# Optimization experiments

Hardware: AMD Instinct MI355X
Metric: run time of the kernel (lower is better)

The kernel has to match this reference:

```python
import jax, jax.numpy as jnp
import numpy as np

EPS = 1e-5


def adder_conv(x, w, stride, padding):
    """AdderNet conv: out[n,o,i,j] = -sum_k |patch[n,i,j,k] - w[o,k]|.
    x: [N, Cin, H, W], w: [Cout, Cin, kh, kw]."""
    Cout, Cin, kh, kw = w.shape
    # patches: [N, Cin*kh*kw, Ho, Wo]
    p = jax.lax.conv_general_dilated_patches(
        x, (kh, kw), (stride, stride), [(padding, padding), (padding, padding)])
    p = jnp.transpose(p, (0, 2, 3, 1))  # [N, Ho, Wo, K]
    wf = w.reshape(Cout, Cin * kh * kw)  # [Cout, K]
    # sequential map over output channels bounds peak memory to one [N,Ho,Wo,K]
    # abs-diff tensor at a time (no huge [N,Cout,Ho,Wo,K] broadcast)
    def one_out(wo):
        return jnp.sum(jnp.abs(p - wo), axis=-1)  # [N, Ho, Wo]
    out = jax.lax.map(one_out, wf)  # [Cout, N, Ho, Wo]
    return -jnp.transpose(out, (1, 0, 2, 3))  # [N, Cout, Ho, Wo]


def bn_relu6(x, gamma, beta):
    # training-mode BatchNorm2d (batch statistics, biased variance) + ReLU6
    mean = jnp.mean(x, axis=(0, 2, 3), keepdims=True)
    var = jnp.var(x, axis=(0, 2, 3), keepdims=True)
    y = (x - mean) * jax.lax.rsqrt(var + EPS)
    y = y * gamma.reshape(1, -1, 1, 1) + beta.reshape(1, -1, 1, 1)
    return jnp.clip(y, 0.0, 6.0)


def setup_inputs() -> dict:
    key = jax.random.key(0)
    ks = jax.random.split(key, 20)
    f32 = jnp.float32

    def wgt(k, shape):
        return jax.random.normal(k, shape, f32) * 0.05

    def bn(k, c):
        k1, k2 = jax.random.split(k)
        g = 1.0 + 0.1 * jax.random.normal(k1, (c,), f32)
        b = 0.1 * jax.random.normal(k2, (c,), f32)
        return g, b

    x = jax.random.normal(ks[0], (16, 512, 38, 38), f32)
    w1 = wgt(ks[1], (256, 512, 1, 1)); g1, b1 = bn(ks[7], 256)
    w2 = wgt(ks[2], (512, 256, 3, 3)); g2, b2 = bn(ks[8], 512)
    w3 = wgt(ks[3], (128, 512, 1, 1)); g3, b3 = bn(ks[9], 128)
    w4 = wgt(ks[4], (256, 128, 3, 3)); g4, b4 = bn(ks[10], 256)
    w5 = wgt(ks[5], (128, 256, 1, 1)); g5, b5 = bn(ks[11], 128)
    w6 = wgt(ks[6], (256, 128, 3, 3)); g6, b6 = bn(ks[12], 256)
    return {"x": x,
            "w1": w1, "g1": g1, "b1": b1,
            "w2": w2, "g2": g2, "b2": b2,
            "w3": w3, "g3": g3, "b3": b3,
            "w4": w4, "g4": g4, "b4": b4,
            "w5": w5, "g5": g5, "b5": b5,
            "w6": w6, "g6": g6, "b6": b6}


def reference(x, w1, g1, b1, w2, g2, b2, w3, g3, b3,
              w4, g4, b4, w5, g5, b5, w6, g6, b6):
    x = bn_relu6(adder_conv(x, w1, 1, 0), g1, b1)  # [N,256,38,38]
    x = bn_relu6(adder_conv(x, w2, 2, 1), g2, b2)  # [N,512,19,19]
    x = bn_relu6(adder_conv(x, w3, 1, 0), g3, b3)  # [N,128,19,19]
    x = bn_relu6(adder_conv(x, w4, 2, 1), g4, b4)  # [N,256,10,10]
    x = bn_relu6(adder_conv(x, w5, 1, 0), g5, b5)  # [N,128,10,10]
    x = bn_relu6(adder_conv(x, w6, 2, 0), g6, b6)  # [N,256,4,4]
    return x
```

## Files before the change

kernel.cpp:

```cpp
#include <hip/hip_runtime.h>


#define QSCALE 131072.0f
#define QBIAS  1048576.5f
#define QINV   7.62939453125e-06

template <bool IS3x3, bool BN>
__global__ __launch_bounds__(256, 4)
void adder_conv(const float* __restrict__ x, const unsigned* __restrict__ wT,
                const float2* __restrict__ ab, unsigned* __restrict__ part,
                int Cin, int H, int W, int Wo, int Cout,
                int stride, int pad, int cpz, int P, int PI, int Pp)
{
    constexpr int KC = 32;
    __shared__ unsigned xs[KC][68];
    __shared__ unsigned ws[KC][128];
    __shared__ float2 abls[512];

    const int t  = threadIdx.x;
    const int tx = t & 15, ty = t >> 4;
    const int ptile = blockIdx.x * 64, otile = blockIdx.y * 128;
    const int pp = t & 63, rg = t >> 6;
    const int oq = t & 31, kr = t >> 5;

    if (BN) {
        for (int i = t; i < Cin; i += 256) abls[i] = ab[i];
        __syncthreads();
    }

    const int p_st = ptile + pp;
    const bool pv = p_st < P;
    int n_st = 0, q = 0;
    if (pv) { n_st = p_st / PI; q = p_st - n_st * PI; }
    const int oh = q / Wo, ow = q - oh * Wo;
    const int ih0 = oh * stride - pad, iw0 = ow * stride - pad;
    const int HWi = H * W;
    const float* xb = x + (size_t)n_st * Cin * HWi;
    const unsigned* wbase = wT + otile + oq * 4;

    unsigned acc[4][8] = {};

    const int chunkBeg = blockIdx.z * cpz, chunkEnd = chunkBeg + cpz;

    float xr0, xr1, xr2, xr3, xr4, xr5, xr6, xr7;
    uint4 wr0, wr1, wr2, wr3;
    int c0P = 0; bool vP = false;

#define ISSUE(CH) do {                                                        \
        const int k0_ = (CH) * KC;                                            \
        int c0_, ih_, iw_;                                                    \
        if (IS3x3) {                                                          \
            const int tap_ = k0_ / Cin;               \
            c0_ = k0_ - tap_ * Cin;                                           \
            const int kh_ = tap_ / 3, kw_ = tap_ - kh_ * 3;                   \
            ih_ = ih0 + kh_; iw_ = iw0 + kw_;                                 \
        } else { c0_ = k0_; ih_ = ih0; iw_ = iw0; }                           \
        vP = pv && (!IS3x3 || (ih_ >= 0 && ih_ < H && iw_ >= 0 && iw_ < W));  \
        c0P = c0_;                                                            \
        const float* px_ = xb + (size_t)(c0_ + rg) * HWi + (ih_ * W + iw_);   \
        xr0 = vP ? px_[0] : 0.f;                                              \
        xr1 = vP ? px_[(size_t) 4 * HWi] : 0.f;                               \
        xr2 = vP ? px_[(size_t) 8 * HWi] : 0.f;                               \
        xr3 = vP ? px_[(size_t)12 * HWi] : 0.f;                               \
        xr4 = vP ? px_[(size_t)16 * HWi] : 0.f;                               \
        xr5 = vP ? px_[(size_t)20 * HWi] : 0.f;                               \
        xr6 = vP ? px_[(size_t)24 * HWi] : 0.f;                               \
        xr7 = vP ? px_[(size_t)28 * HWi] : 0.f;                               \
        const unsigned* pw_ = wbase + (size_t)(k0_ + kr) * Cout;              \
        wr0 = *(const uint4*)(pw_);                                           \
        wr1 = *(const uint4*)(pw_ + (size_t) 8 * Cout);                       \
        wr2 = *(const uint4*)(pw_ + (size_t)16 * Cout);                       \
        wr3 = *(const uint4*)(pw_ + (size_t)24 * Cout);                       \
    } while (0)

#define BNQ(V, J, DST)                                                        \
        {                                                                     \
            float vv_ = V;                                                    \
            if (BN) {                                                         \
                const float2 s_ = abls[c0P + rg + 4 * (J)];                   \
                vv_ = fminf(fmaxf(fmaf(s_.x, vv_, s_.y), 0.f), 6.f);          \
                vv_ = vP ? vv_ : 0.f;            \
            }                                                                 \
            DST = (unsigned)fmaf(vv_, QSCALE, QBIAS);                         \
        }

#define WRITE_LDS() do {                                                      \
        unsigned q0_, q1_, q2_, q3_, q4_, q5_, q6_, q7_;                      \
        BNQ(xr0, 0, q0_) BNQ(xr1, 1, q1_) BNQ(xr2, 2, q2_) BNQ(xr3, 3, q3_)   \
        BNQ(xr4, 4, q4_) BNQ(xr5, 5, q5_) BNQ(xr6, 6, q6_) BNQ(xr7, 7, q7_)   \
        xs[rg     ][pp] = q0_; xs[rg +  4][pp] = q1_;                         \
        xs[rg +  8][pp] = q2_; xs[rg + 12][pp] = q3_;                         \
        xs[rg + 16][pp] = q4_; xs[rg + 20][pp] = q5_;                         \
        xs[rg + 24][pp] = q6_; xs[rg + 28][pp] = q7_;                         \
        *(uint4*)&ws[kr     ][oq * 4] = wr0;                                  \
        *(uint4*)&ws[kr +  8][oq * 4] = wr1;                                  \
        *(uint4*)&ws[kr + 16][oq * 4] = wr2;                                  \
        *(uint4*)&ws[kr + 24][oq * 4] = wr3;                                  \
    } while (0)

    ISSUE(chunkBeg);

    for (int ch = chunkBeg; ch < chunkEnd; ++ch) {
        WRITE_LDS();
        if (ch + 1 < chunkEnd) ISSUE(ch + 1);
        asm volatile("s_waitcnt lgkmcnt(0)" ::: "memory");
        __builtin_amdgcn_s_barrier();
        asm volatile("" ::: "memory");

#pragma unroll 2
        for (int kk = 0; kk < KC; ++kk) {
            const uint4 xv = *(const uint4*)&xs[kk][tx * 4];
            const uint4 wa = *(const uint4*)&ws[kk][ty * 8];
            const uint4 wb = *(const uint4*)&ws[kk][ty * 8 + 4];
#define S1(A, XC, WC) asm("v_sad_u32 %0, %1, %2, %0" : "+v"(A) : "v"(XC), "v"(WC));
#define SROW(I, XC)                                             \
            S1(acc[I][0], XC, wa.x) S1(acc[I][1], XC, wa.y)     \
            S1(acc[I][2], XC, wa.z) S1(acc[I][3], XC, wa.w)     \
            S1(acc[I][4], XC, wb.x) S1(acc[I][5], XC, wb.y)     \
            S1(acc[I][6], XC, wb.z) S1(acc[I][7], XC, wb.w)
            SROW(0, xv.x) SROW(1, xv.y) SROW(2, xv.z) SROW(3, xv.w)
#undef SROW
#undef S1
        }
        asm volatile("" ::: "memory");
        __builtin_amdgcn_s_barrier();
        asm volatile("" ::: "memory");
    }
#undef ISSUE
#undef BNQ
#undef WRITE_LDS

    const int p0 = ptile + tx * 4;
    const bool full = (p0 + 3) < P;
#pragma unroll
    for (int jj = 0; jj < 8; ++jj) {
        const int o = otile + ty * 8 + jj;
        unsigned* dst = part + ((size_t)blockIdx.z * Cout + o) * Pp + p0;
        if (full) {
            *(uint4*)dst = make_uint4(acc[0][jj], acc[1][jj], acc[2][jj], acc[3][jj]);
        } else {
#pragma unroll
            for (int i = 0; i < 4; ++i)
                if (p0 + i < P) dst[i] = acc[i][jj];
        }
    }
}

__global__ void combine_stats(const unsigned* __restrict__ part, float* __restrict__ fin,
                              double* __restrict__ st, int C, int PI, int Z, int Pp)
{
    const int c = blockIdx.x, n = blockIdx.y, t = threadIdx.x;
    const int pbase = n * PI;
    double s = 0.0, s2 = 0.0;
    for (int qq = t; qq < PI; qq += 256) {
        unsigned long long u = 0;
        for (int z = 0; z < Z; ++z)
            u += part[((size_t)z * C + c) * Pp + pbase + qq];
        const float v = -(float)((double)u * QINV);
        fin[((size_t)n * C + c) * PI + qq] = v;
        s += v; s2 += (double)v * v;
    }
    __shared__ double sh[256], sh2[256];
    sh[t] = s; sh2[t] = s2; __syncthreads();
    for (int off = 128; off > 0; off >>= 1) {
        if (t < off) { sh[t] += sh[t + off]; sh2[t] += sh2[t + off]; }
        __syncthreads();
    }
    if (t == 0) {
        unsafeAtomicAdd(&st[2 * c], sh[0]);
        unsafeAtomicAdd(&st[2 * c + 1], sh2[0]);
    }
}

__global__ void ab_kernel(const double* __restrict__ st, const float* __restrict__ gamma,
                          const float* __restrict__ beta, float2* __restrict__ ab,
                          int C, double invCount)
{
    const int c = blockIdx.x * blockDim.x + threadIdx.x;
    if (c < C) {
        const double mean = st[2 * c] * invCount;
        const double var  = st[2 * c + 1] * invCount - mean * mean;
        const float a = gamma[c] * rsqrtf((float)var + 1e-5f);
        const float b = beta[c] - (float)mean * a;
        ab[c] = make_float2(a, b);
    }
}

__global__ void apply_kernel(const float* __restrict__ y, const float2* __restrict__ ab,
                             float* __restrict__ out, int total, int C, int PI)
{
    const int i = blockIdx.x * 256 + threadIdx.x;
    if (i < total) {
        const int c = (i / PI) % C;
        const float2 s = ab[c];
        out[i] = fminf(fmaxf(fmaf(s.x, y[i], s.y), 0.f), 6.f);
    }
}

struct TDesc { const float* w; unsigned* wT; int Cout; int Cin; int Tap; int elems; };
struct TPack { TDesc d[6]; };

__global__ void transpose_all(TPack p)
{
    const TDesc d = p.d[blockIdx.y];
    const int i = blockIdx.x * 256 + threadIdx.x;
    if (i < d.elems) {
        const int k = i / d.Cout, o = i - k * d.Cout;
        const int tap = k / d.Cin, c = k - tap * d.Cin;
        const float v = d.w[((size_t)o * d.Cin + c) * d.Tap + tap];
        d.wT[i] = (unsigned)fmaf(v, QSCALE, QBIAS);
    }
}

extern "C" void kernel_launch(void* const* d_in, const int* in_sizes, int n_in,
                              void* d_out, int out_size, void* d_ws, size_t ws_size,
                              hipStream_t stream)
{
    const float* x = (const float*)d_in[0];
    const float *w[6], *g[6], *bt[6];
    for (int i = 0; i < 6; ++i) {
        w[i]  = (const float*)d_in[1 + 3 * i];
        g[i]  = (const float*)d_in[2 + 3 * i];
        bt[i] = (const float*)d_in[3 + 3 * i];
    }

    char* ws = (char*)d_ws;
    float* bufA = (float*)ws;
    float* bufB = (float*)(ws + 23658496);
    unsigned* part = (unsigned*)(ws + 23658496 + 11829248);
    size_t off = 23658496 + 11829248 + 23658496;
    const int wElems[6] = {256 * 512, 512 * 2304, 128 * 512,
                           256 * 1152, 128 * 256, 256 * 1152};
    unsigned* wT[6];
    for (int i = 0; i < 6; ++i) { wT[i] = (unsigned*)(ws + off); off += (size_t)wElems[i] * 4; }
    double* st = (double*)(ws + off); off += 3072 * 8;
    float2* ab = (float2*)(ws + off);
    const int stOff[6] = {0, 512, 1536, 1792, 2304, 2560};
    const int abOff[6] = {0, 256, 768, 896, 1152, 1280};

    const dim3 blk(256);

    hipMemsetAsync(st, 0, 3072 * 8, stream);

    TPack tp;
    const int wCout[6] = {256, 512, 128, 256, 128, 256};
    const int wCin[6]  = {512, 256, 512, 128, 256, 128};
    const int wTap[6]  = {1, 9, 1, 9, 1, 9};
    for (int i = 0; i < 6; ++i)
        tp.d[i] = TDesc{w[i], wT[i], wCout[i], wCin[i], wTap[i], wElems[i]};
    transpose_all<<<dim3((1179648 + 255) / 256, 6), blk, 0, stream>>>(tp);

    adder_conv<false, false><<<dim3(361, 2, 1), blk, 0, stream>>>(
        x, wT[0], nullptr, part, 512, 38, 38, 38, 256, 1, 0, 16, 23104, 1444, 23104);
    combine_stats<<<dim3(256, 16), blk, 0, stream>>>(part, bufA, st + stOff[0], 256, 1444, 1, 23104);
    ab_kernel<<<1, blk, 0, stream>>>(st + stOff[0], g[0], bt[0], ab + abOff[0], 256, 1.0 / 23104);

    adder_conv<true, true><<<dim3(91, 4, 2), blk, 0, stream>>>(
        bufA, wT[1], ab + abOff[0], part, 256, 38, 38, 19, 512, 2, 1, 36, 5776, 361, 5776);
    combine_stats<<<dim3(512, 16), blk, 0, stream>>>(part, bufB, st + stOff[1], 512, 361, 2, 5776);
    ab_kernel<<<2, blk, 0, stream>>>(st + stOff[1], g[1], bt[1], ab + abOff[1], 512, 1.0 / 5776);

    adder_conv<false, true><<<dim3(91, 1, 8), blk, 0, stream>>>(
        bufB, wT[2], ab + abOff[1], part, 512, 19, 19, 19, 128, 1, 0, 2, 5776, 361, 5776);
    combine_stats<<<dim3(128, 16), blk, 0, stream>>>(part, bufA, st + stOff[2], 128, 361, 8, 5776);
    ab_kernel<<<1, blk, 0, stream>>>(st + stOff[2], g[2], bt[2], ab + abOff[2], 128, 1.0 / 5776);

    adder_conv<true, true><<<dim3(25, 2, 12), blk, 0, stream>>>(
        bufA, wT[3], ab + abOff[2], part, 128, 19, 19, 10, 256, 2, 1, 3, 1600, 100, 1600);
    combine_stats<<<dim3(256, 16), blk, 0, stream>>>(part, bufB, st + stOff[3], 256, 100, 12, 1600);
    ab_kernel<<<1, blk, 0, stream>>>(st + stOff[3], g[3], bt[3], ab + abOff[3], 256, 1.0 / 1600);

    adder_conv<false, true><<<dim3(25, 1, 8), blk, 0, stream>>>(
        bufB, wT[4], ab + abOff[3], part, 256, 10, 10, 10, 128, 1, 0, 1, 1600, 100, 1600);
    combine_stats<<<dim3(128, 16), blk, 0, stream>>>(part, bufA, st + stOff[4], 128, 100, 8, 1600);
    ab_kernel<<<1, blk, 0, stream>>>(st + stOff[4], g[4], bt[4], ab + abOff[4], 128, 1.0 / 1600);

    adder_conv<true, true><<<dim3(4, 2, 18), blk, 0, stream>>>(
        bufA, wT[5], ab + abOff[4], part, 128, 10, 10, 4, 256, 2, 0, 2, 256, 16, 256);
    combine_stats<<<dim3(256, 16), blk, 0, stream>>>(part, bufB, st + stOff[5], 256, 16, 18, 256);
    ab_kernel<<<1, blk, 0, stream>>>(st + stOff[5], g[5], bt[5], ab + abOff[5], 256, 1.0 / 256);

    apply_kernel<<<(65536 + 255) / 256, blk, 0, stream>>>(bufB, ab + abOff[5], (float*)d_out,
                                                          65536, 256, 16);
}
```

Measured before the change: 668.8 us.

## Enlarge adder-conv pixel tile to 128 with split 2x4x8 register microtile

Doubles the pixel tile per block from 64 to 128 and gives each thread a 2x4x8 accumulator block built from two split x and w sub-tiles. This lowers the LDS reads per v_sad op and halves the grid size in the pixel dimension. The cost is more registers per thread (launch bounds lowered to 3 blocks), fewer blocks to fill the GPU, and more waste on the tail tiles of small layers.

```diff
diff --git a/kernel.cpp b/kernel.cpp
--- a/kernel.cpp
+++ b/kernel.cpp
@@ -6,21 +6,21 @@
 #define QINV   7.62939453125e-06
 
 template <bool IS3x3, bool BN>
-__global__ __launch_bounds__(256, 4)
+__global__ __launch_bounds__(256, 3)
 void adder_conv(const float* __restrict__ x, const unsigned* __restrict__ wT,
                 const float2* __restrict__ ab, unsigned* __restrict__ part,
                 int Cin, int H, int W, int Wo, int Cout,
                 int stride, int pad, int cpz, int P, int PI, int Pp)
 {
     constexpr int KC = 32;
-    __shared__ unsigned xs[KC][68];
+    __shared__ unsigned xs[KC][132];
     __shared__ unsigned ws[KC][128];
     __shared__ float2 abls[512];
 
     const int t  = threadIdx.x;
     const int tx = t & 15, ty = t >> 4;
-    const int ptile = blockIdx.x * 64, otile = blockIdx.y * 128;
-    const int pp = t & 63, rg = t >> 6;
+    const int ptile = blockIdx.x * 128, otile = blockIdx.y * 128;
+    const int pp = t & 127, rg = t >> 7;
     const int oq = t & 31, kr = t >> 5;
 
     if (BN) {
@@ -38,11 +38,12 @@
     const float* xb = x + (size_t)n_st * Cin * HWi;
     const unsigned* wbase = wT + otile + oq * 4;
 
-    unsigned acc[4][8] = {};
+    unsigned acc[2][4][8] = {};
 
     const int chunkBeg = blockIdx.z * cpz, chunkEnd = chunkBeg + cpz;
 
     float xr0, xr1, xr2, xr3, xr4, xr5, xr6, xr7;
+    float xr8, xr9, xr10, xr11, xr12, xr13, xr14, xr15;
     uint4 wr0, wr1, wr2, wr3;
     int c0P = 0; bool vP = false;
 
@@ -50,7 +51,7 @@
         const int k0_ = (CH) * KC;                                            \
         int c0_, ih_, iw_;                                                    \
         if (IS3x3) {                                                          \
-            const int tap_ = k0_ / Cin;               \
+            const int tap_ = k0_ / Cin;                \
             c0_ = k0_ - tap_ * Cin;                                           \
             const int kh_ = tap_ / 3, kw_ = tap_ - kh_ * 3;                   \
             ih_ = ih0 + kh_; iw_ = iw0 + kw_;                                 \
@@ -58,14 +59,22 @@
         vP = pv && (!IS3x3 || (ih_ >= 0 && ih_ < H && iw_ >= 0 && iw_ < W));  \
         c0P = c0_;                                                            \
         const float* px_ = xb + (size_t)(c0_ + rg) * HWi + (ih_ * W + iw_);   \
-        xr0 = vP ? px_[0] : 0.f;                                              \
-        xr1 = vP ? px_[(size_t) 4 * HWi] : 0.f;                               \
-        xr2 = vP ? px_[(size_t) 8 * HWi] : 0.f;                               \
-        xr3 = vP ? px_[(size_t)12 * HWi] : 0.f;                               \
-        xr4 = vP ? px_[(size_t)16 * HWi] : 0.f;                               \
-        xr5 = vP ? px_[(size_t)20 * HWi] : 0.f;                               \
-        xr6 = vP ? px_[(size_t)24 * HWi] : 0.f;                               \
-        xr7 = vP ? px_[(size_t)28 * HWi] : 0.f;                               \
+        xr0  = vP ? px_[0] : 0.f;                                             \
+        xr1  = vP ? px_[(size_t) 2 * HWi] : 0.f;                              \
+        xr2  = vP ? px_[(size_t) 4 * HWi] : 0.f;                              \
+        xr3  = vP ? px_[(size_t) 6 * HWi] : 0.f;                              \
+        xr4  = vP ? px_[(size_t) 8 * HWi] : 0.f;                              \
+        xr5  = vP ? px_[(size_t)10 * HWi] : 0.f;                              \
+        xr6  = vP ? px_[(size_t)12 * HWi] : 0.f;                              \
+        xr7  = vP ? px_[(size_t)14 * HWi] : 0.f;                              \
+        xr8  = vP ? px_[(size_t)16 * HWi] : 0.f;                              \
+        xr9  = vP ? px_[(size_t)18 * HWi] : 0.f;                              \
+        xr10 = vP ? px_[(size_t)20 * HWi] : 0.f;                              \
+        xr11 = vP ? px_[(size_t)22 * HWi] : 0.f;                              \
+        xr12 = vP ? px_[(size_t)24 * HWi] : 0.f;                              \
+        xr13 = vP ? px_[(size_t)26 * HWi] : 0.f;                              \
+        xr14 = vP ? px_[(size_t)28 * HWi] : 0.f;                              \
+        xr15 = vP ? px_[(size_t)30 * HWi] : 0.f;                              \
         const unsigned* pw_ = wbase + (size_t)(k0_ + kr) * Cout;              \
         wr0 = *(const uint4*)(pw_);                                           \
         wr1 = *(const uint4*)(pw_ + (size_t) 8 * Cout);                       \
@@ -77,7 +86,7 @@
         {                                                                     \
             float vv_ = V;                                                    \
             if (BN) {                                                         \
-                const float2 s_ = abls[c0P + rg + 4 * (J)];                   \
+                const float2 s_ = abls[c0P + rg + 2 * (J)];                   \
                 vv_ = fminf(fmaxf(fmaf(s_.x, vv_, s_.y), 0.f), 6.f);          \
                 vv_ = vP ? vv_ : 0.f;            \
             }                                                                 \
@@ -86,12 +95,19 @@
 
 #define WRITE_LDS() do {                                                      \
         unsigned q0_, q1_, q2_, q3_, q4_, q5_, q6_, q7_;                      \
-        BNQ(xr0, 0, q0_) BNQ(xr1, 1, q1_) BNQ(xr2, 2, q2_) BNQ(xr3, 3, q3_)   \
-        BNQ(xr4, 4, q4_) BNQ(xr5, 5, q5_) BNQ(xr6, 6, q6_) BNQ(xr7, 7, q7_)   \
-        xs[rg     ][pp] = q0_; xs[rg +  4][pp] = q1_;                         \
-        xs[rg +  8][pp] = q2_; xs[rg + 12][pp] = q3_;                         \
-        xs[rg + 16][pp] = q4_; xs[rg + 20][pp] = q5_;                         \
-        xs[rg + 24][pp] = q6_; xs[rg + 28][pp] = q7_;                         \
+        unsigned q8_, q9_, qA_, qB_, qC_, qD_, qE_, qF_;                      \
+        BNQ(xr0,  0, q0_) BNQ(xr1,  1, q1_) BNQ(xr2,  2, q2_) BNQ(xr3,  3, q3_) \
+        BNQ(xr4,  4, q4_) BNQ(xr5,  5, q5_) BNQ(xr6,  6, q6_) BNQ(xr7,  7, q7_) \
+        BNQ(xr8,  8, q8_) BNQ(xr9,  9, q9_) BNQ(xr10,10, qA_) BNQ(xr11,11, qB_) \
+        BNQ(xr12,12, qC_) BNQ(xr13,13, qD_) BNQ(xr14,14, qE_) BNQ(xr15,15, qF_) \
+        xs[rg     ][pp] = q0_; xs[rg +  2][pp] = q1_;                         \
+        xs[rg +  4][pp] = q2_; xs[rg +  6][pp] = q3_;                         \
+        xs[rg +  8][pp] = q4_; xs[rg + 10][pp] = q5_;                         \
+        xs[rg + 12][pp] = q6_; xs[rg + 14][pp] = q7_;                         \
+        xs[rg + 16][pp] = q8_; xs[rg + 18][pp] = q9_;                         \
+        xs[rg + 20][pp] = qA_; xs[rg + 22][pp] = qB_;                         \
+        xs[rg + 24][pp] = qC_; xs[rg + 26][pp] = qD_;                         \
+        xs[rg + 28][pp] = qE_; xs[rg + 30][pp] = qF_;                         \
         *(uint4*)&ws[kr     ][oq * 4] = wr0;                                  \
         *(uint4*)&ws[kr +  8][oq * 4] = wr1;                                  \
         *(uint4*)&ws[kr + 16][oq * 4] = wr2;                                  \
@@ -109,16 +125,18 @@
 
 #pragma unroll 2
         for (int kk = 0; kk < KC; ++kk) {
-            const uint4 xv = *(const uint4*)&xs[kk][tx * 4];
-            const uint4 wa = *(const uint4*)&ws[kk][ty * 8];
-            const uint4 wb = *(const uint4*)&ws[kk][ty * 8 + 4];
+            const uint4 xa = *(const uint4*)&xs[kk][tx * 4];
+            const uint4 xb2 = *(const uint4*)&xs[kk][64 + tx * 4];
+            const uint4 wa = *(const uint4*)&ws[kk][ty * 4];
+            const uint4 wb = *(const uint4*)&ws[kk][64 + ty * 4];
 #define S1(A, XC, WC) asm("v_sad_u32 %0, %1, %2, %0" : "+v"(A) : "v"(XC), "v"(WC));
-#define SROW(I, XC)                                             \
-            S1(acc[I][0], XC, wa.x) S1(acc[I][1], XC, wa.y)     \
-            S1(acc[I][2], XC, wa.z) S1(acc[I][3], XC, wa.w)     \
-            S1(acc[I][4], XC, wb.x) S1(acc[I][5], XC, wb.y)     \
-            S1(acc[I][6], XC, wb.z) S1(acc[I][7], XC, wb.w)
-            SROW(0, xv.x) SROW(1, xv.y) SROW(2, xv.z) SROW(3, xv.w)
+#define SROW(a, i, XC)                                            \
+            S1(acc[a][i][0], XC, wa.x) S1(acc[a][i][1], XC, wa.y) \
+            S1(acc[a][i][2], XC, wa.z) S1(acc[a][i][3], XC, wa.w) \
+            S1(acc[a][i][4], XC, wb.x) S1(acc[a][i][5], XC, wb.y) \
+            S1(acc[a][i][6], XC, wb.z) S1(acc[a][i][7], XC, wb.w)
+            SROW(0, 0, xa.x) SROW(0, 1, xa.y) SROW(0, 2, xa.z) SROW(0, 3, xa.w)
+            SROW(1, 0, xb2.x) SROW(1, 1, xb2.y) SROW(1, 2, xb2.z) SROW(1, 3, xb2.w)
 #undef SROW
 #undef S1
         }
@@ -130,18 +148,22 @@
 #undef BNQ
 #undef WRITE_LDS
 
-    const int p0 = ptile + tx * 4;
-    const bool full = (p0 + 3) < P;
 #pragma unroll
-    for (int jj = 0; jj < 8; ++jj) {
-        const int o = otile + ty * 8 + jj;
-        unsigned* dst = part + ((size_t)blockIdx.z * Cout + o) * Pp + p0;
-        if (full) {
-            *(uint4*)dst = make_uint4(acc[0][jj], acc[1][jj], acc[2][jj], acc[3][jj]);
-        } else {
+    for (int a = 0; a < 2; ++a) {
+        const int p0 = ptile + a * 64 + tx * 4;
+        const bool full = (p0 + 3) < P;
 #pragma unroll
-            for (int i = 0; i < 4; ++i)
-                if (p0 + i < P) dst[i] = acc[i][jj];
+        for (int jj = 0; jj < 8; ++jj) {
+            const int o = otile + (jj < 4 ? ty * 4 + jj : 64 + ty * 4 + (jj - 4));
+            unsigned* dst = part + ((size_t)blockIdx.z * Cout + o) * Pp + p0;
+            if (full) {
+                *(uint4*)dst = make_uint4(acc[a][0][jj], acc[a][1][jj],
+                                          acc[a][2][jj], acc[a][3][jj]);
+            } else {
+#pragma unroll
+                for (int i = 0; i < 4; ++i)
+                    if (p0 + i < P) dst[i] = acc[a][i][jj];
+            }
         }
     }
 }
@@ -250,32 +272,32 @@
         tp.d[i] = TDesc{w[i], wT[i], wCout[i], wCin[i], wTap[i], wElems[i]};
     transpose_all<<<dim3((1179648 + 255) / 256, 6), blk, 0, stream>>>(tp);
 
-    adder_conv<false, false><<<dim3(361, 2, 1), blk, 0, stream>>>(
+    adder_conv<false, false><<<dim3(181, 2, 1), blk, 0, stream>>>(
         x, wT[0], nullptr, part, 512, 38, 38, 38, 256, 1, 0, 16, 23104, 1444, 23104);
     combine_stats<<<dim3(256, 16), blk, 0, stream>>>(part, bufA, st + stOff[0], 256, 1444, 1, 23104);
     ab_kernel<<<1, blk, 0, stream>>>(st + stOff[0], g[0], bt[0], ab + abOff[0], 256, 1.0 / 23104);
 
-    adder_conv<true, true><<<dim3(91, 4, 2), blk, 0, stream>>>(
+    adder_conv<true, true><<<dim3(46, 4, 2), blk, 0, stream>>>(
         bufA, wT[1], ab + abOff[0], part, 256, 38, 38, 19, 512, 2, 1, 36, 5776, 361, 5776);
     combine_stats<<<dim3(512, 16), blk, 0, stream>>>(part, bufB, st + stOff[1], 512, 361, 2, 5776);
     ab_kernel<<<2, blk, 0, stream>>>(st + stOff[1], g[1], bt[1], ab + abOff[1], 512, 1.0 / 5776);
 
-    adder_conv<false, true><<<dim3(91, 1, 8), blk, 0, stream>>>(
+    adder_conv<false, true><<<dim3(46, 1, 8), blk, 0, stream>>>(
         bufB, wT[2], ab + abOff[1], part, 512, 19, 19, 19, 128, 1, 0, 2, 5776, 361, 5776);
     combine_stats<<<dim3(128, 16), blk, 0, stream>>>(part, bufA, st + stOff[2], 128, 361, 8, 5776);
     ab_kernel<<<1, blk, 0, stream>>>(st + stOff[2], g[2], bt[2], ab + abOff[2], 128, 1.0 / 5776);
 
-    adder_conv<true, true><<<dim3(25, 2, 12), blk, 0, stream>>>(
+    adder_conv<true, true><<<dim3(13, 2, 12), blk, 0, stream>>>(
         bufA, wT[3], ab + abOff[2], part, 128, 19, 19, 10, 256, 2, 1, 3, 1600, 100, 1600);
     combine_stats<<<dim3(256, 16), blk, 0, stream>>>(part, bufB, st + stOff[3], 256, 100, 12, 1600);
     ab_kernel<<<1, blk, 0, stream>>>(st + stOff[3], g[3], bt[3], ab + abOff[3], 256, 1.0 / 1600);
 
-    adder_conv<false, true><<<dim3(25, 1, 8), blk, 0, stream>>>(
+    adder_conv<false, true><<<dim3(13, 1, 8), blk, 0, stream>>>(
         bufB, wT[4], ab + abOff[3], part, 256, 10, 10, 10, 128, 1, 0, 1, 1600, 100, 1600);
     combine_stats<<<dim3(128, 16), blk, 0, stream>>>(part, bufA, st + stOff[4], 128, 100, 8, 1600);
     ab_kernel<<<1, blk, 0, stream>>>(st + stOff[4], g[4], bt[4], ab + abOff[4], 128, 1.0 / 1600);
 
-    adder_conv<true, true><<<dim3(4, 2, 18), blk, 0, stream>>>(
+    adder_conv<true, true><<<dim3(2, 2, 18), blk, 0, stream>>>(
         bufA, wT[5], ab + abOff[4], part, 128, 10, 10, 4, 256, 2, 0, 2, 256, 16, 256);
     combine_stats<<<dim3(256, 16), blk, 0, stream>>>(part, bufB, st + stOff[5], 256, 16, 18, 256);
     ab_kernel<<<1, blk, 0, stream>>>(st + stOff[5], g[5], bt[5], ab + abOff[5], 256, 1.0 / 256);
```

Measured after the change: 804.8 us. 1.2x slower.
